# Performance work log

Hardware: AMD Instinct MI355X
Metric: run time of the kernel (lower is better)

## Reference

```python
import jax, jax.numpy as jnp
import numpy as np

NUM_EMBEDDINGS = 512
EMBEDDING_DIM = 64
COMMITMENT_COST = 0.25


def setup_inputs() -> dict:
    key = jax.random.key(0)
    k1, k2 = jax.random.split(key)
    inputs = jax.random.normal(k1, (16, EMBEDDING_DIM, 4096), dtype=jnp.float32)
    # torch init: uniform(-1/num_embeddings, 1/num_embeddings)
    codebook = jax.random.uniform(
        k2, (NUM_EMBEDDINGS, EMBEDDING_DIM), dtype=jnp.float32,
        minval=-1.0 / NUM_EMBEDDINGS, maxval=1.0 / NUM_EMBEDDINGS)
    return {"inputs": inputs, "codebook": codebook}


def reference(inputs, codebook):
    # inputs: [B, D, T] -> permute to [B, T, D]
    x = jnp.transpose(inputs, (0, 2, 1))
    B, T, D = x.shape
    K = codebook.shape[0]
    flat = x.reshape(-1, D)  # [N, D]

    distances = (jnp.sum(flat * flat, axis=1, keepdims=True)
                 + jnp.sum(codebook * codebook, axis=1)
                 - 2.0 * flat @ codebook.T)  # [N, K]
    idx = jnp.argmin(distances, axis=1)  # [N]
    encodings = jax.nn.one_hot(idx, K, dtype=jnp.float32)  # [N, K]

    # direct gather == encodings @ codebook
    quantized = codebook[idx].reshape(B, T, D)

    e_latent_loss = jnp.mean((jax.lax.stop_gradient(quantized) - x) ** 2)
    q_latent_loss = jnp.mean((quantized - jax.lax.stop_gradient(x)) ** 2)
    loss = q_latent_loss + COMMITMENT_COST * e_latent_loss

    # straight-through estimator
    quantized_st = x + jax.lax.stop_gradient(quantized - x)

    avg_probs = jnp.mean(encodings, axis=0)
    perplexity = jnp.exp(-jnp.sum(avg_probs * jnp.log(avg_probs + 1e-10)))

    return (loss, jnp.transpose(quantized_st, (0, 2, 1)), perplexity, encodings)
```

## Files before the change

### kernel.cpp

```cpp
#include <hip/hip_runtime.h>

#define B_ 16
#define D_ 64
#define T_ 4096
#define K_ 512
#define N_ (B_*T_)
#define Q_ (B_*D_*T_)
#define ENC_OFF ((size_t)(2 + Q_))

#define WS_LOSS    0
#define WS_HIST    16
#define WS_NE      2064
#define WS_CBH     4608
#define WS_CBL     70144

typedef __bf16 bf16x8 __attribute__((ext_vector_type(8)));
typedef float  f32x4  __attribute__((ext_vector_type(4)));

__global__ __launch_bounds__(256) void k0_init(const float* __restrict__ cb,
                                               float* __restrict__ ne,
                                               int* __restrict__ hist,
                                               double* __restrict__ loss,
                                               bf16x8* __restrict__ cbh,
                                               bf16x8* __restrict__ cbl) {
    int bidx = blockIdx.x, tid = threadIdx.x;

    if (tid < 64) {
        int code = bidx * 64 + tid;
        float s = 0.f;
#pragma unroll
        for (int d = 0; d < 64; ++d) { float c = cb[code*64 + d]; s = fmaf(c, c, s); }
        ne[code] = s;
    }
    if (bidx == 0) {
        hist[tid] = 0; hist[tid + 256] = 0;
        if (tid == 0) *loss = 0.0;
    }

#pragma unroll
    for (int p = 0; p < 2; ++p) {
        int e = p * 256 + tid;
        int ct = bidx * 4 + (e >> 7);
        int ks = (e >> 6) & 1;
        int lane = e & 63;
        int code  = ct * 16 + (lane & 15);
        int dbase = ks * 32 + ((lane >> 4) << 3);
        bf16x8 h, l;
#pragma unroll
        for (int j = 0; j < 8; ++j) {
            float v = cb[code * 64 + dbase + j];
            __bf16 hv = (__bf16)v;
            __bf16 lv = (__bf16)(v - (float)hv);
            h[j] = hv; l[j] = lv;
        }
        cbh[(ct * 2 + ks) * 64 + lane] = h;
        cbl[(ct * 2 + ks) * 64 + lane] = l;
    }
}

__global__ __launch_bounds__(256) void k_main(const float* __restrict__ in,
                                              const float* __restrict__ cb,
                                              const bf16x8* __restrict__ cbh,
                                              const bf16x8* __restrict__ cbl,
                                              const float* __restrict__ ne,
                                              float* __restrict__ out,
                                              float2* __restrict__ enc2,
                                              int* __restrict__ hist,
                                              double* __restrict__ loss) {
    __shared__ float X[64][65];
    __shared__ float ne_s[512];
    __shared__ int   sidx[64];
    int tid = threadIdx.x;
    int n0 = blockIdx.x * 64;
    int b  = n0 >> 12, t0 = n0 & (T_ - 1);

    {
        int tl = tid & 63, dg = tid >> 6;
#pragma unroll
        for (int i = 0; i < 16; ++i) {
            int d = dg * 16 + i;
            X[d][tl] = in[((size_t)b * 64 + d) * T_ + t0 + tl];
        }
    }
    ne_s[tid] = ne[tid];
    ne_s[tid + 256] = ne[tid + 256];
    __syncthreads();

    int w = tid >> 6, lane = tid & 63;
    int col = lane & 15, q = lane >> 4;

    bf16x8 Ah[2], Al[2];
#pragma unroll
    for (int ks = 0; ks < 2; ++ks) {
        bf16x8 h, l;
#pragma unroll
        for (int j = 0; j < 8; ++j) {
            float v = X[ks * 32 + q * 8 + j][w * 16 + col];
            __bf16 hv = (__bf16)v;
            __bf16 lv = (__bf16)(v - (float)hv);
            h[j] = hv; l[j] = lv;
        }
        Ah[ks] = h; Al[ks] = l;
    }

    float m1[4]; int i1[4];
#pragma unroll
    for (int e = 0; e < 4; ++e) { m1[e] = 3.4e38f; i1[e] = 0; }

    for (int ct = 0; ct < 32; ++ct) {
        bf16x8 Bh0 = cbh[(ct * 2 + 0) * 64 + lane];
        bf16x8 Bh1 = cbh[(ct * 2 + 1) * 64 + lane];
        bf16x8 Bl0 = cbl[(ct * 2 + 0) * 64 + lane];
        bf16x8 Bl1 = cbl[(ct * 2 + 1) * 64 + lane];
        float nev = ne_s[ct * 16 + col];
        int code = ct * 16 + col;
        f32x4 acc = {0.f, 0.f, 0.f, 0.f};
        acc = __builtin_amdgcn_mfma_f32_16x16x32_bf16(Ah[0], Bh0, acc, 0, 0, 0);
        acc = __builtin_amdgcn_mfma_f32_16x16x32_bf16(Ah[1], Bh1, acc, 0, 0, 0);
        acc = __builtin_amdgcn_mfma_f32_16x16x32_bf16(Ah[0], Bl0, acc, 0, 0, 0);
        acc = __builtin_amdgcn_mfma_f32_16x16x32_bf16(Al[0], Bh0, acc, 0, 0, 0);
        acc = __builtin_amdgcn_mfma_f32_16x16x32_bf16(Ah[1], Bl1, acc, 0, 0, 0);
        acc = __builtin_amdgcn_mfma_f32_16x16x32_bf16(Al[1], Bh1, acc, 0, 0, 0);
#pragma unroll
        for (int e = 0; e < 4; ++e) {
            float sc = fmaf(-2.f, acc[e], nev);
            bool lt = sc < m1[e];
            i1[e] = lt ? code : i1[e];
            m1[e] = lt ? sc : m1[e];
        }
    }

#pragma unroll
    for (int e = 0; e < 4; ++e) {
        float a1 = m1[e]; int ai = i1[e];
#pragma unroll
        for (int off = 1; off < 16; off <<= 1) {
            float o1 = __shfl_xor(a1, off);
            int   oi = __shfl_xor(ai, off);
            bool tk = (o1 < a1) || (o1 == a1 && oi < ai);
            a1 = tk ? o1 : a1; ai = tk ? oi : ai;
        }
        if (col == 0) sidx[w * 16 + q * 4 + e] = ai;
    }
    __syncthreads();

#pragma unroll 4
    for (int i = 0; i < 64; ++i) {
        int id = sidx[i];
        float2 v;
        v.x = ((id >> 1) == tid && (id & 1) == 0) ? 1.f : 0.f;
        v.y = ((id >> 1) == tid && (id & 1) == 1) ? 1.f : 0.f;
        enc2[(size_t)(n0 + i) * 256 + tid] = v;
    }

    int tl = tid & 63, dg = tid >> 6;
    int idq = sidx[tl];
    const float4* cq4 = (const float4*)(cb + (size_t)idq * 64 + dg * 16);
    float* qp = out + 1 + (size_t)b * D_ * T_ + (size_t)(dg * 16) * T_ + t0 + tl;

    float lsum = 0.f;
#pragma unroll
    for (int j4 = 0; j4 < 4; ++j4) {
        float4 qv = cq4[j4];
        float qe[4] = {qv.x, qv.y, qv.z, qv.w};
#pragma unroll
        for (int e = 0; e < 4; ++e) {
            int dl = j4 * 4 + e;
            float xv = X[dg * 16 + dl][tl];
            float diff = qe[e] - xv;
            lsum = fmaf(diff, diff, lsum);
            qp[(size_t)dl * T_] = xv + diff;
        }
    }
    if (tid < 64) atomicAdd(&hist[idq], 1);

#pragma unroll
    for (int off = 32; off > 0; off >>= 1) lsum += __shfl_down(lsum, off);
    __shared__ float wsum[4];
    if ((tid & 63) == 0) wsum[tid >> 6] = lsum;
    __syncthreads();
    if (tid == 0) {
        double s = (double)wsum[0] + (double)wsum[1] + (double)wsum[2] + (double)wsum[3];
        atomicAdd(loss, s);
    }
}

__global__ __launch_bounds__(512) void k6_final(const int* __restrict__ hist,
                                                const double* __restrict__ loss,
                                                float* __restrict__ out) {
    __shared__ double sh[512];
    int k = threadIdx.x;
    double p = (double)hist[k] / (double)N_;
    sh[k] = p * log(p + 1e-10);
    __syncthreads();
    for (int s = 256; s > 0; s >>= 1) {
        if (k < s) sh[k] += sh[k + s];
        __syncthreads();
    }
    if (k == 0) {
        out[1 + Q_] = (float)exp(-sh[0]);
        out[0] = (float)(1.25 * (*loss) / (double)Q_);
    }
}

extern "C" void kernel_launch(void* const* d_in, const int* in_sizes, int n_in,
                              void* d_out, int out_size, void* d_ws, size_t ws_size,
                              hipStream_t stream) {
    const float* in = (const float*)d_in[0];
    const float* cb = (const float*)d_in[1];
    float* out = (float*)d_out;
    char* ws = (char*)d_ws;

    double* loss  = (double*)(ws + WS_LOSS);
    int* hist     = (int*)(ws + WS_HIST);
    float* ne     = (float*)(ws + WS_NE);
    bf16x8* cbh   = (bf16x8*)(ws + WS_CBH);
    bf16x8* cbl   = (bf16x8*)(ws + WS_CBL);

    float2* enc2 = (float2*)(out + ENC_OFF);

    k0_init<<<8, 256, 0, stream>>>(cb, ne, hist, loss, cbh, cbl);
    k_main<<<N_ / 64, 256, 0, stream>>>(in, cb, cbh, cbl, ne, out, enc2, hist, loss);
    k6_final<<<1, 512, 0, stream>>>(hist, loss, out);
}
```

Before: 197.3 us.

## Fuse final reduction via ticket, add nontemporal loads/stores, vectorize input load

Removes the separate final kernel by having the last block, chosen through an atomic ticket, compute the perplexity and the loss. Input loads become vectorized float4 nontemporal loads with a new thread-to-element mapping, and the large encodings and quantized outputs use nontemporal stores. The init kernel is spread over 16 blocks, and k_main gets a launch-bounds occupancy hint. The ticket scheme adds a fence and an atomic per block, and writes to X in shared memory may now see bank conflicts with the new mapping.

Result: slower. 256.1 us (+29.8%).

```diff
diff --git a/kernel.cpp b/kernel.cpp
--- a/kernel.cpp
+++ b/kernel.cpp
@@ -9,6 +9,7 @@
 #define ENC_OFF ((size_t)(2 + Q_))
 
 #define WS_LOSS    0
+#define WS_TICKET  8
 #define WS_HIST    16
 #define WS_NE      2064
 #define WS_CBH     4608
@@ -16,57 +17,56 @@
 
 typedef __bf16 bf16x8 __attribute__((ext_vector_type(8)));
 typedef float  f32x4  __attribute__((ext_vector_type(4)));
+typedef float  f32x2  __attribute__((ext_vector_type(2)));
 
 __global__ __launch_bounds__(256) void k0_init(const float* __restrict__ cb,
                                                float* __restrict__ ne,
                                                int* __restrict__ hist,
                                                double* __restrict__ loss,
+                                               int* __restrict__ ticket,
                                                bf16x8* __restrict__ cbh,
                                                bf16x8* __restrict__ cbl) {
     int bidx = blockIdx.x, tid = threadIdx.x;
 
-    if (tid < 64) {
-        int code = bidx * 64 + tid;
+    {
+        int code = bidx * 32 + (tid >> 3), sl = tid & 7;
         float s = 0.f;
 #pragma unroll
-        for (int d = 0; d < 64; ++d) { float c = cb[code*64 + d]; s = fmaf(c, c, s); }
-        ne[code] = s;
+        for (int j = 0; j < 8; ++j) { float c = cb[code * 64 + sl * 8 + j]; s = fmaf(c, c, s); }
+        s += __shfl_xor(s, 1); s += __shfl_xor(s, 2); s += __shfl_xor(s, 4);
+        if (sl == 0) ne[code] = s;
     }
     if (bidx == 0) {
         hist[tid] = 0; hist[tid + 256] = 0;
-        if (tid == 0) *loss = 0.0;
-    }
-
-#pragma unroll
-    for (int p = 0; p < 2; ++p) {
-        int e = p * 256 + tid;
-        int ct = bidx * 4 + (e >> 7);
-        int ks = (e >> 6) & 1;
-        int lane = e & 63;
-        int code  = ct * 16 + (lane & 15);
-        int dbase = ks * 32 + ((lane >> 4) << 3);
-        bf16x8 h, l;
-#pragma unroll
-        for (int j = 0; j < 8; ++j) {
-            float v = cb[code * 64 + dbase + j];
-            __bf16 hv = (__bf16)v;
-            __bf16 lv = (__bf16)(v - (float)hv);
-            h[j] = hv; l[j] = lv;
-        }
-        cbh[(ct * 2 + ks) * 64 + lane] = h;
-        cbl[(ct * 2 + ks) * 64 + lane] = l;
-    }
+        if (tid == 0) { *loss = 0.0; *ticket = 0; }
+    }
+
+    int e = bidx * 256 + tid;
+    int ct = e >> 7, ks = (e >> 6) & 1, lane = e & 63;
+    int code  = ct * 16 + (lane & 15);
+    int dbase = ks * 32 + ((lane >> 4) << 3);
+    bf16x8 h, l;
+#pragma unroll
+    for (int j = 0; j < 8; ++j) {
+        float v = cb[code * 64 + dbase + j];
+        __bf16 hv = (__bf16)v;
+        __bf16 lv = (__bf16)(v - (float)hv);
+        h[j] = hv; l[j] = lv;
+    }
+    cbh[(ct * 2 + ks) * 64 + lane] = h;
+    cbl[(ct * 2 + ks) * 64 + lane] = l;
 }
 
-__global__ __launch_bounds__(256) void k_main(const float* __restrict__ in,
-                                              const float* __restrict__ cb,
-                                              const bf16x8* __restrict__ cbh,
-                                              const bf16x8* __restrict__ cbl,
-                                              const float* __restrict__ ne,
-                                              float* __restrict__ out,
-                                              float2* __restrict__ enc2,
-                                              int* __restrict__ hist,
-                                              double* __restrict__ loss) {
+__global__ __launch_bounds__(256, 4) void k_main(const float* __restrict__ in,
+                                                 const float* __restrict__ cb,
+                                                 const bf16x8* __restrict__ cbh,
+                                                 const bf16x8* __restrict__ cbl,
+                                                 const float* __restrict__ ne,
+                                                 float* __restrict__ out,
+                                                 f32x2* __restrict__ enc2,
+                                                 int* __restrict__ hist,
+                                                 double* __restrict__ loss,
+                                                 int* __restrict__ ticket) {
     __shared__ float X[64][65];
     __shared__ float ne_s[512];
     __shared__ int   sidx[64];
@@ -75,11 +75,15 @@
     int b  = n0 >> 12, t0 = n0 & (T_ - 1);
 
     {
-        int tl = tid & 63, dg = tid >> 6;
-#pragma unroll
-        for (int i = 0; i < 16; ++i) {
-            int d = dg * 16 + i;
-            X[d][tl] = in[((size_t)b * 64 + d) * T_ + t0 + tl];
+        int d = tid >> 2, qd = tid & 3;
+        const f32x4* ip = (const f32x4*)(in + ((size_t)b * 64 + d) * T_ + t0 + qd * 16);
+#pragma unroll
+        for (int j = 0; j < 4; ++j) {
+            f32x4 v = __builtin_nontemporal_load(&ip[j]);
+            X[d][qd * 16 + j * 4 + 0] = v[0];
+            X[d][qd * 16 + j * 4 + 1] = v[1];
+            X[d][qd * 16 + j * 4 + 2] = v[2];
+            X[d][qd * 16 + j * 4 + 3] = v[3];
         }
     }
     ne_s[tid] = ne[tid];
@@ -147,10 +151,10 @@
 #pragma unroll 4
     for (int i = 0; i < 64; ++i) {
         int id = sidx[i];
-        float2 v;
-        v.x = ((id >> 1) == tid && (id & 1) == 0) ? 1.f : 0.f;
-        v.y = ((id >> 1) == tid && (id & 1) == 1) ? 1.f : 0.f;
-        enc2[(size_t)(n0 + i) * 256 + tid] = v;
+        f32x2 v;
+        v[0] = ((id >> 1) == tid && (id & 1) == 0) ? 1.f : 0.f;
+        v[1] = ((id >> 1) == tid && (id & 1) == 1) ? 1.f : 0.f;
+        __builtin_nontemporal_store(v, &enc2[(size_t)(n0 + i) * 256 + tid]);
     }
 
     int tl = tid & 63, dg = tid >> 6;
@@ -169,7 +173,7 @@
             float xv = X[dg * 16 + dl][tl];
             float diff = qe[e] - xv;
             lsum = fmaf(diff, diff, lsum);
-            qp[(size_t)dl * T_] = xv + diff;
+            __builtin_nontemporal_store(xv + diff, &qp[(size_t)dl * T_]);
         }
     }
     if (tid < 64) atomicAdd(&hist[idq], 1);
@@ -177,29 +181,35 @@
 #pragma unroll
     for (int off = 32; off > 0; off >>= 1) lsum += __shfl_down(lsum, off);
     __shared__ float wsum[4];
+    __shared__ int lastflag;
     if ((tid & 63) == 0) wsum[tid >> 6] = lsum;
     __syncthreads();
     if (tid == 0) {
         double s = (double)wsum[0] + (double)wsum[1] + (double)wsum[2] + (double)wsum[3];
         atomicAdd(loss, s);
-    }
-}
-
-__global__ __launch_bounds__(512) void k6_final(const int* __restrict__ hist,
-                                                const double* __restrict__ loss,
-                                                float* __restrict__ out) {
-    __shared__ double sh[512];
-    int k = threadIdx.x;
-    double p = (double)hist[k] / (double)N_;
-    sh[k] = p * log(p + 1e-10);
-    __syncthreads();
-    for (int s = 256; s > 0; s >>= 1) {
-        if (k < s) sh[k] += sh[k + s];
+        __threadfence();
+        int t = atomicAdd(ticket, 1);
+        lastflag = (t == (N_ / 64) - 1);
+    }
+    __syncthreads();
+
+    if (lastflag) {
+        int h0 = atomicAdd(&hist[tid], 0);
+        int h1 = atomicAdd(&hist[tid + 256], 0);
+        double p0 = (double)h0 / (double)N_;
+        double p1 = (double)h1 / (double)N_;
+        double lp = p0 * log(p0 + 1e-10) + p1 * log(p1 + 1e-10);
+#pragma unroll
+        for (int off = 32; off > 0; off >>= 1) lp += __shfl_down(lp, off);
+        __shared__ double dsum[4];
+        if ((tid & 63) == 0) dsum[tid >> 6] = lp;
         __syncthreads();
-    }
-    if (k == 0) {
-        out[1 + Q_] = (float)exp(-sh[0]);
-        out[0] = (float)(1.25 * (*loss) / (double)Q_);
+        if (tid == 0) {
+            double s = dsum[0] + dsum[1] + dsum[2] + dsum[3];
+            double L = atomicAdd(loss, 0.0);
+            out[1 + Q_] = (float)exp(-s);
+            out[0] = (float)(1.25 * L / (double)Q_);
+        }
     }
 }
 
@@ -212,14 +222,14 @@
     char* ws = (char*)d_ws;
 
     double* loss  = (double*)(ws + WS_LOSS);
+    int* ticket   = (int*)(ws + WS_TICKET);
     int* hist     = (int*)(ws + WS_HIST);
     float* ne     = (float*)(ws + WS_NE);
     bf16x8* cbh   = (bf16x8*)(ws + WS_CBH);
     bf16x8* cbl   = (bf16x8*)(ws + WS_CBL);
 
-    float2* enc2 = (float2*)(out + ENC_OFF);
-
-    k0_init<<<8, 256, 0, stream>>>(cb, ne, hist, loss, cbh, cbl);
-    k_main<<<N_ / 64, 256, 0, stream>>>(in, cb, cbh, cbl, ne, out, enc2, hist, loss);
-    k6_final<<<1, 512, 0, stream>>>(hist, loss, out);
+    f32x2* enc2 = (f32x2*)(out + ENC_OFF);
+
+    k0_init<<<16, 256, 0, stream>>>(cb, ne, hist, loss, ticket, cbh, cbl);
+    k_main<<<N_ / 64, 256, 0, stream>>>(in, cb, cbh, cbl, ne, out, enc2, hist, loss, ticket);
 }
```
